# Performance work log

Measured on AMD Instinct MI355X. Metric: run time of the kernel, lower is better.

The kernel has to match this reference:

```python
import jax, jax.numpy as jnp
import numpy as np

B, L, N, CIN = 16, 12, 2048, 3
EMB, GRAP, LAYERS, OUT = 64, 16, 3, 12
SP, TID, DIW = 16, 16, 16
M = EMB + SP + TID + DIW  # model_size = 112


def setup_inputs() -> dict:
    key = jax.random.key(0)
    ks = jax.random.split(key, 12)
    s = jnp.float32(0.02)
    return {
        "history_data": jax.random.uniform(ks[0], (B, L, N, CIN), dtype=jnp.float32),
        "adj": jax.nn.softmax(jax.random.normal(ks[1], (N, N), dtype=jnp.float32), axis=1),
        "node_emb": jax.random.normal(ks[2], (N, SP), dtype=jnp.float32) * s,
        "tid_emb": jax.random.normal(ks[3], (288, TID), dtype=jnp.float32) * s,
        "diw_emb": jax.random.normal(ks[4], (7, DIW), dtype=jnp.float32) * s,
        "W_in": jax.random.normal(ks[5], (CIN, EMB), dtype=jnp.float32) * s,
        "b_in": jnp.zeros((EMB,), jnp.float32),
        "W_pre": jax.random.normal(ks[6], (M, 4 * M), dtype=jnp.float32) * s,
        "b_pre": jnp.zeros((4 * M,), jnp.float32),
        "E_dy": jax.random.normal(ks[7], (N, GRAP), dtype=jnp.float32) * s,
        "W_dy": jax.random.normal(ks[8], (M, 4 * M), dtype=jnp.float32) * s,
        "b_dy": jnp.zeros((4 * M,), jnp.float32),
        "W_dec": jax.random.normal(ks[9], (OUT, LAYERS, M), dtype=jnp.float32) * s,
        "b_dec": jnp.zeros((OUT,), jnp.float32),
        "W_out": jax.random.normal(ks[10], (OUT, OUT), dtype=jnp.float32) * s,
        "b_out": jnp.zeros((OUT,), jnp.float32),
    }


def _run_layer(hidd_t, A, W, b):
    """Graph-conv LSTM-style recurrent layer; returns last-timestep hidden [B,N,M]."""
    def step(ct, x):  # x: [B,N,M]
        xa = jnp.einsum('bkm,nk->bnm', x, A)      # adjacency message passing
        gates = xa @ W + b                         # [B,N,4M]
        i, f, g, o = jnp.split(gates, 4, axis=-1)
        ct = jax.nn.sigmoid(f) * ct + jax.nn.sigmoid(i) * jnp.tanh(g)
        ht = jax.nn.sigmoid(o) * jnp.tanh(ct)
        return ct, ht
    ct0 = jnp.zeros(hidd_t.shape[1:], hidd_t.dtype)  # [B,N,M]
    _, hts = jax.lax.scan(step, ct0, hidd_t)
    return hts[-1]


def reference(history_data, adj, node_emb, tid_emb, diw_emb, W_in, b_in,
              W_pre, b_pre, E_dy, W_dy, b_dy, W_dec, b_dec, W_out, b_out):
    Bx, Lx = history_data.shape[0], history_data.shape[1]
    # temporal embedding indices (truncating cast, matches torch LongTensor)
    t_idx = (history_data[..., 1] * 288).astype(jnp.int32)
    d_idx = (history_data[..., 2] * 7).astype(jnp.int32)
    inp = history_data @ W_in + b_in                                   # [B,L,N,EMB]
    node = jnp.broadcast_to(node_emb, (Bx, Lx) + node_emb.shape)       # [B,L,N,SP]
    hidd = jnp.concatenate([inp, node, tid_emb[t_idx], diw_emb[d_idx]], axis=-1)  # [B,L,N,M]
    hidd_t = jnp.moveaxis(hidd, 1, 0)                                  # [L,B,N,M]
    A_dy = jax.nn.softmax(jax.nn.relu(E_dy @ E_dy.T), axis=1)          # adaptive adjacency
    outs = [_run_layer(hidd_t, adj, W_pre, b_pre)]                     # layer 0: predefined graph
    for _ in range(LAYERS - 1):
        outs.append(_run_layer(hidd_t, A_dy, W_dy, b_dy))              # layers >0: dynamic graph
    final = jnp.stack(outs, axis=1)                                    # [B,LAYERS,N,M]
    # decoder Conv2d(layer_num->out_len, kernel (1,M)) then 1x1 Conv2d
    x = jnp.einsum('bznm,ozm->bon', final, W_dec) + b_dec[None, :, None]
    x = jnp.einsum('bon,po->bpn', x, W_out) + b_out[None, :, None]
    return x  # [B,OUT,N]
```

## Files before the change

kernel.cpp:

```cpp
#include <hip/hip_runtime.h>
#include <hip/hip_bf16.h>
#include <cstdint>
#include <cstddef>

typedef float f4 __attribute__((ext_vector_type(4)));
typedef short s16x8 __attribute__((ext_vector_type(8)));
typedef short s16x4 __attribute__((ext_vector_type(4)));

#define N_NODES 2048
#define BATCH 16
#define LSEQ 12
#define MDIM 112
#define GDIM 448
#define KC 35
#define NCOLS_X 6784
#define NREAL (KC*BATCH*LSEQ)
#define XROW 7680
#define KBIG 2048
#define KL 64
#define WTB_SH (GDIM * KL)

#define GLDS16(SRC, DST)                                                        \
    __builtin_amdgcn_global_load_lds(                                           \
        (const __attribute__((address_space(1))) void*)(SRC),                   \
        (__attribute__((address_space(3))) void*)(DST), 16, 0, 0)

#define MFMA16(ACC, AV, BV) \
    ACC = __builtin_amdgcn_mfma_f32_16x16x32_bf16(AV, BV, ACC, 0, 0, 0)

__device__ __forceinline__ short bf16hi(float v) {
    union { __hip_bfloat16 h; short s; } u;
    u.h = __float2bfloat16(v);
    return u.s;
}
__device__ __forceinline__ short bf16lo(float v) {
    union { __hip_bfloat16 h; short s; } u;
    u.h = __float2bfloat16(v);
    float r = v - __bfloat162float(u.h);
    u.h = __float2bfloat16(r);
    return u.s;
}
__device__ __forceinline__ float rcpf_(float x)  { return __builtin_amdgcn_rcpf(x); }
__device__ __forceinline__ float sigf_(float x)  { return rcpf_(1.0f + __expf(-x)); }
__device__ __forceinline__ float tanhf_(float x) { return 1.0f - 2.0f * rcpf_(1.0f + __expf(2.0f * x)); }

__device__ __forceinline__ float wave_sum(float v) {
#pragma unroll
    for (int off = 32; off > 0; off >>= 1) v += __shfl_down(v, off);
    return v;
}

__global__ void adaptive_adj_kernel(const float* __restrict__ E,
                                    const float* __restrict__ node_emb,
                                    __hip_bfloat16* __restrict__ Abig,
                                    float* __restrict__ node_a,
                                    float* __restrict__ rs)
{
    __shared__ float sbuf[N_NODES];
    __shared__ float red[256];
    __shared__ float part[17][4];
    const int n = blockIdx.x;
    const int tid = threadIdx.x;
    float en[16];
#pragma unroll
    for (int i = 0; i < 16; ++i) en[i] = E[n * 16 + i];
    float lmax = -3.4e38f;
    for (int k = tid; k < N_NODES; k += 256) {
        const float* ek = E + k * 16;
        float d = 0.f;
#pragma unroll
        for (int i = 0; i < 16; ++i) d += en[i] * ek[i];
        d = fmaxf(d, 0.0f);
        sbuf[k] = d;
        lmax = fmaxf(lmax, d);
    }
    red[tid] = lmax; __syncthreads();
    for (int s = 128; s > 0; s >>= 1) {
        if (tid < s) red[tid] = fmaxf(red[tid], red[tid + s]);
        __syncthreads();
    }
    float mx = red[0];
    __syncthreads();
    float lsum = 0.f;
    for (int k = tid; k < N_NODES; k += 256) {
        float e = __expf(sbuf[k] - mx);
        sbuf[k] = e;
        lsum += e;
    }
    red[tid] = lsum; __syncthreads();
    for (int s = 128; s > 0; s >>= 1) {
        if (tid < s) red[tid] += red[tid + s];
        __syncthreads();
    }
    float rinv = rcpf_(red[0]);
    __syncthreads();

    __hip_bfloat16* arow = Abig + (size_t)(2048 + n) * KBIG;
    float p[17];
#pragma unroll
    for (int i = 0; i < 17; ++i) p[i] = 0.f;
    for (int k = tid; k < N_NODES; k += 256) {
        float a = sbuf[k] * rinv;
        arow[k] = __float2bfloat16(a);
        const float* e = node_emb + k * 16;
        p[16] += a;
#pragma unroll
        for (int i = 0; i < 16; ++i) p[i] += a * e[i];
    }
#pragma unroll
    for (int e = 0; e < 17; ++e) {
        float v = wave_sum(p[e]);
        if ((tid & 63) == 0) part[e][tid >> 6] = v;
    }
    __syncthreads();
    if (tid < 17) {
        float s = part[tid][0] + part[tid][1] + part[tid][2] + part[tid][3];
        if (tid < 16) node_a[n * 16 + tid] = s;
        else rs[n] = s;
    }
}

__global__ void node_rs_kernel(const float* __restrict__ A,
                               const float* __restrict__ node_emb,
                               float* __restrict__ node_a, float* __restrict__ rs)
{
    __shared__ float part[17][4];
    const int n = blockIdx.x;
    const int tid = threadIdx.x;
    float p[17];
#pragma unroll
    for (int i = 0; i < 17; ++i) p[i] = 0.f;
    for (int k = tid; k < N_NODES; k += 256) {
        float a = A[(size_t)n * N_NODES + k];
        const float* e = node_emb + k * 16;
        p[16] += a;
#pragma unroll
        for (int i = 0; i < 16; ++i) p[i] += a * e[i];
    }
#pragma unroll
    for (int e = 0; e < 17; ++e) {
        float v = wave_sum(p[e]);
        if ((tid & 63) == 0) part[e][tid >> 6] = v;
    }
    __syncthreads();
    if (tid < 17) {
        float s = part[tid][0] + part[tid][1] + part[tid][2] + part[tid][3];
        if (tid < 16) node_a[n * 16 + tid] = s;
        else rs[n] = s;
    }
}

__global__ void wtb_pack_kernel(const float* __restrict__ W_in,
                                const float* __restrict__ b_in,
                                const float* __restrict__ Wp,
                                const float* __restrict__ bp,
                                const float* __restrict__ Wd,
                                const float* __restrict__ bd,
                                short* __restrict__ outp)
{
    int idx = blockIdx.x * 256 + threadIdx.x;
    if (idx >= 2 * GDIM * KL) return;
    int z = idx >= GDIM * KL;
    int rem = idx - z * GDIM * KL;
    const float* W  = z ? Wd : Wp;
    const float* bg = z ? bd : bp;
    int p = rem & 63;
    int r = rem >> 6;
    int tile = r >> 4, gc = r & 15;
    int mi = tile >> 2, co = tile & 3;
    int g = co * 112 + mi * 16 + gc;

    float v = 0.f; bool lo = false; bool zero = false;
    #define DOTW(VEC) ({ float s_ = 0.f;                                     \
        for (int m = 0; m < 64; ++m) s_ += (VEC)[m] * W[(size_t)m * GDIM + g];\
        s_; })
    if (p < 3)         v = DOTW(W_in + p * 64);
    else if (p < 35)   v = W[(size_t)(80 + p - 3) * GDIM + g];
    else if (p < 38)   v = DOTW(W_in + (p - 35) * 64);
    else if (p < 41) { v = DOTW(W_in + (p - 38) * 64); lo = true; }
    else if (p == 41)  v = bg[g];
    else if (p == 42)  v = DOTW(b_in);
    else if (p < 59)   v = W[(size_t)(64 + p - 43) * GDIM + g];
    else if (p == 59) { v = bg[g]; lo = true; }
    else if (p == 60) { v = DOTW(b_in); lo = true; }
    else zero = true;
    #undef DOTW
    short s = zero ? (short)0 : (lo ? bf16lo(v) : bf16hi(v));
    int a = r * 128 + p * 2;
    int asw = a ^ (((a >> 7) & 7) << 4);
    outp[(size_t)z * WTB_SH + (asw >> 1)] = s;
}

#define AQUADS (2048 * 2048 / 4)
#define XQUADS (NCOLS_X * 2048 / 4)
__global__ void pack_build_kernel(const float* __restrict__ adj,
                                  const float* __restrict__ hist,
                                  const float* __restrict__ tid_emb,
                                  const float* __restrict__ diw_emb,
                                  __hip_bfloat16* __restrict__ Abig,
                                  __hip_bfloat16* __restrict__ XT)
{
    int idx = blockIdx.x * 256 + threadIdx.x;
    if (idx < AQUADS) {
        int e0 = idx << 2;
        int k = e0 & 2047;
        int m = e0 >> 11;
        f4 v = *(const f4*)(adj + (size_t)m * 2048 + k);
        s16x4 o = { bf16hi(v[0]), bf16hi(v[1]), bf16hi(v[2]), bf16hi(v[3]) };
        *(s16x4*)((short*)Abig + (size_t)m * KBIG + k) = o;
        return;
    }
    int xi = idx - AQUADS;
    if (xi >= XQUADS) return;
    int e0 = xi << 2;
    int k0 = e0 & 2047;
    int jl = e0 >> 11;
    s16x4 o = {0, 0, 0, 0};
    if (jl < NREAL) {
        int c = jl % KC;
        int bl = jl / KC;
#pragma unroll
        for (int i = 0; i < 4; ++i) {
            const float* h = hist + ((size_t)(bl * N_NODES + k0 + i)) * 3;
            float v;
            if (c < 3) v = h[c];
            else if (c < 19) { int ti = (int)(h[1] * 288.0f); v = tid_emb[ti * 16 + (c - 3)]; }
            else             { int di = (int)(h[2] * 7.0f);   v = diw_emb[di * 16 + (c - 19)]; }
            o[i] = bf16hi(v);
        }
    }
    *(s16x4*)((short*)XT + (size_t)jl * KBIG + k0) = o;
}

__global__ __launch_bounds__(512, 4) void gemm_bf16_kernel(const short* __restrict__ A,
                                                           const short* __restrict__ BT,
                                                           short* __restrict__ XAhi)
{
    __shared__ short As[256 * 64];
    __shared__ short Bs[128 * 64];
    const int tid = threadIdx.x;
    const int w = tid >> 6;
    const int l = tid & 63;
    const int wr = w >> 1;
    const int wc = w & 1;
    const int lm = l & 15;

    const int bid = blockIdx.y * 53 + blockIdx.x;
    const int sid = (bid & 7) * 106 + (bid >> 3);
    const int col = sid >> 4;
    const int row = sid & 15;
    const int m0 = row * 256;
    const int jt = col * 128;

    const int srow = tid >> 3;
    const int koct = (tid & 7) ^ (srow & 7);
    const size_t gA = (size_t)(m0 + srow) * KBIG + koct * 8;
    const size_t gB = (size_t)(jt + srow) * KBIG + koct * 8;
    char* lA = (char*)As + srow * 128 + (tid & 7) * 16;
    char* lB = (char*)Bs + srow * 128 + (tid & 7) * 16;

    f4 acc[4][4];
#pragma unroll
    for (int i = 0; i < 4; ++i)
#pragma unroll
        for (int j = 0; j < 4; ++j)
#pragma unroll
            for (int e = 0; e < 4; ++e) acc[i][j][e] = 0.f;

    const int sm  = (l & 7) << 4;
    const int k16 = (l >> 4) * 16;

    for (int kt = 0; kt < KBIG; kt += 64) {
        __syncthreads();
        GLDS16(A  + gA + kt,                      lA);
        GLDS16(A  + gA + kt + (size_t)64  * KBIG, lA + 64  * 128);
        GLDS16(A  + gA + kt + (size_t)128 * KBIG, lA + 128 * 128);
        GLDS16(A  + gA + kt + (size_t)192 * KBIG, lA + 192 * 128);
        GLDS16(BT + gB + kt,                      lB);
        GLDS16(BT + gB + kt + (size_t)64  * KBIG, lB + 64  * 128);
        __syncthreads();
#pragma unroll
        for (int ks = 0; ks < 2; ++ks) {
            const int ko = (ks * 64 + k16) ^ sm;
            s16x8 a[4], b[4];
#pragma unroll
            for (int mi = 0; mi < 4; ++mi)
                a[mi] = *(const s16x8*)((const char*)As + (wr * 64 + mi * 16 + lm) * 128 + ko);
#pragma unroll
            for (int ni = 0; ni < 4; ++ni)
                b[ni] = *(const s16x8*)((const char*)Bs + (wc * 64 + ni * 16 + lm) * 128 + ko);
#pragma unroll
            for (int mi = 0; mi < 4; ++mi)
#pragma unroll
                for (int ni = 0; ni < 4; ++ni)
                    MFMA16(acc[mi][ni], a[mi], b[ni]);
        }
    }

    const int rbase = m0 + wr * 64 + (l >> 4) * 4;
    const int cbase = jt + wc * 64 + lm;
#pragma unroll
    for (int mi = 0; mi < 4; ++mi)
#pragma unroll
        for (int ni = 0; ni < 4; ++ni) {
            int cc = cbase + ni * 16;
            if (cc < NREAL) {
                int bt = cc / KC;
                int c  = cc - bt * KC;
#pragma unroll
                for (int reg = 0; reg < 4; ++reg) {
                    size_t roff = (size_t)(rbase + mi * 16 + reg) * XROW;
                    float v = acc[mi][ni][reg];
                    XAhi[roff + (size_t)bt * 40 + c] = bf16hi(v);
                    if (c < 3) XAhi[roff + (size_t)bt * 40 + 36 + c] = bf16lo(v);
                }
            }
        }
}

__global__ __launch_bounds__(512, 4) void lstm6_kernel(
    const short* __restrict__ XAhi,
    const short* __restrict__ WtBg,
    const float* __restrict__ na_pre, const float* __restrict__ na_dy,
    const float* __restrict__ rs_pre, const float* __restrict__ rs_dy,
    float* __restrict__ H)
{
    __shared__ short sWtb[WTB_SH];
    __shared__ short sXa[128 * KL];
    const int tid = threadIdx.x;
    const int w = tid >> 6, l = tid & 63;
    const int n0 = blockIdx.x * 128;
    const int b  = blockIdx.y;
    const int z  = blockIdx.z;
    const float* na = z ? na_dy : na_pre;
    const float* rs = z ? rs_dy : rs_pre;

    {
        const char* gW = (const char*)(WtBg + (size_t)z * WTB_SH);
        char* lW = (char*)sWtb;
        for (int it = 0; it < 7; ++it) {
            int base = (it * 8 + w) * 64;
            GLDS16(gW + (size_t)(base + l) * 16, lW + base * 16);
        }
    }

    const int sr = tid & 127;
    const int pp = tid >> 7;
    const short* xarow = XAhi + (size_t)(z * 2048 + n0 + sr) * XROW;
    const float* narow = na + (size_t)(n0 + sr) * 16;
    const float rsv = rs[n0 + sr];
    char* wrow = (char*)sXa + sr * 128;
    const int wswz = (sr & 7) << 4;

    const int lm = l & 15;
    const int sm = (l & 7) << 4;
    const int kof0 = ((l >> 4) * 16) ^ sm;
    const int kof1 = (64 + (l >> 4) * 16) ^ sm;
    const int an = w * 16 + lm;
    const char* xab = (const char*)sXa;
    const char* wtbb = (const char*)sWtb;
    float* Hout = H + (size_t)z * BATCH * N_NODES * MDIM;

    float cc[7][4];
#pragma unroll
    for (int mi = 0; mi < 7; ++mi)
#pragma unroll
        for (int q = 0; q < 4; ++q) cc[mi][q] = 0.f;

    s16x8 ph0 = {0,0,0,0,0,0,0,0}, ph1 = ph0;
    s16x4 p0 = {0,0,0,0}, p32 = p0, plo = p0;
    {
        const int bt = b * LSEQ;
        if (pp < 2) {
            ph0 = *(const s16x8*)(xarow + bt * 40 + pp * 16);
            ph1 = *(const s16x8*)(xarow + bt * 40 + pp * 16 + 8);
        } else if (pp == 2) {
            p0  = *(const s16x4*)(xarow + bt * 40);
            p32 = *(const s16x4*)(xarow + bt * 40 + 32);
            plo = *(const s16x4*)(xarow + bt * 40 + 36);
        }
    }

    for (int t = 0; t < LSEQ; ++t) {
        __syncthreads();
        if (pp < 2) {
            *(s16x8*)(wrow + ((pp * 32 + 0)  ^ wswz)) = ph0;
            *(s16x8*)(wrow + ((pp * 32 + 16) ^ wswz)) = ph1;
        } else if (pp == 2) {
            short v[16];
            v[0] = p32[0]; v[1] = p32[1]; v[2] = p32[2];
            v[3] = plo[0]; v[4] = plo[1]; v[5] = plo[2];
            v[6] = p0[0];  v[7] = p0[1];  v[8] = p0[2];
            v[9]  = bf16hi(1.0f);
            v[10] = bf16hi(rsv);
#pragma unroll
            for (int j = 11; j < 16; ++j) v[j] = bf16hi(narow[j - 11]);
#pragma unroll
            for (int q = 0; q < 4; ++q) {
                s16x4 sv = { v[q * 4], v[q * 4 + 1], v[q * 4 + 2], v[q * 4 + 3] };
                *(s16x4*)(wrow + ((2 * 32 + q * 8) ^ wswz)) = sv;
            }
        } else {
            short v[16];
#pragma unroll
            for (int j = 0; j < 11; ++j) v[j] = bf16hi(narow[5 + j]);
            v[11] = bf16hi(1.0f);
            v[12] = bf16hi(rsv);
            v[13] = 0; v[14] = 0; v[15] = 0;
#pragma unroll
            for (int q = 0; q < 4; ++q) {
                s16x4 sv = { v[q * 4], v[q * 4 + 1], v[q * 4 + 2], v[q * 4 + 3] };
                *(s16x4*)(wrow + ((3 * 32 + q * 8) ^ wswz)) = sv;
            }
        }
        __syncthreads();

        if (t + 1 < LSEQ) {
            const int bt = b * LSEQ + t + 1;
            if (pp < 2) {
                ph0 = *(const s16x8*)(xarow + bt * 40 + pp * 16);
                ph1 = *(const s16x8*)(xarow + bt * 40 + pp * 16 + 8);
            } else if (pp == 2) {
                p0  = *(const s16x4*)(xarow + bt * 40);
                p32 = *(const s16x4*)(xarow + bt * 40 + 32);
                plo = *(const s16x4*)(xarow + bt * 40 + 36);
            }
        }

        s16x8 a0 = *(const s16x8*)(xab + an * 128 + kof0);
        s16x8 a1 = *(const s16x8*)(xab + an * 128 + kof1);
#pragma unroll
        for (int mi = 0; mi < 7; ++mi) {
            const char* bb = wtbb + (mi * 64 + lm) * 128;
            f4 gi = {0.f, 0.f, 0.f, 0.f};
            f4 gf = gi, gg = gi;
            MFMA16(gi, a0, *(const s16x8*)(bb + kof0));
            MFMA16(gi, a1, *(const s16x8*)(bb + kof1));
            MFMA16(gf, a0, *(const s16x8*)(bb + 2048 + kof0));
            MFMA16(gf, a1, *(const s16x8*)(bb + 2048 + kof1));
            MFMA16(gg, a0, *(const s16x8*)(bb + 4096 + kof0));
            MFMA16(gg, a1, *(const s16x8*)(bb + 4096 + kof1));
#pragma unroll
            for (int q = 0; q < 4; ++q) {
                float si = sigf_(gi[q]);
                float sf = sigf_(gf[q]);
                float tg = tanhf_(gg[q]);
                cc[mi][q] = sf * cc[mi][q] + si * tg;
            }
            if (t == LSEQ - 1) {
                f4 go = {0.f, 0.f, 0.f, 0.f};
                MFMA16(go, a0, *(const s16x8*)(bb + 6144 + kof0));
                MFMA16(go, a1, *(const s16x8*)(bb + 6144 + kof1));
#pragma unroll
                for (int q = 0; q < 4; ++q) {
                    float h = sigf_(go[q]) * tanhf_(cc[mi][q]);
                    Hout[((size_t)b * N_NODES + n0 + w * 16 + (l >> 4) * 4 + q) * MDIM
                         + mi * 16 + lm] = h;
                }
            }
        }
    }
}

__global__ void decode_kernel(const float* __restrict__ H,
                              const float* __restrict__ Wdec,
                              const float* __restrict__ bdec,
                              const float* __restrict__ Wout,
                              const float* __restrict__ bout,
                              float* __restrict__ out)
{
    int g = blockIdx.x * 256 + threadIdx.x;
    if (g >= BATCH * N_NODES) return;
    int b = g >> 11;
    int n = g & 2047;
    const f4* h0 = (const f4*)(H + (size_t)g * MDIM);
    const f4* h1 = (const f4*)(H + (size_t)BATCH * N_NODES * MDIM + (size_t)g * MDIM);
    float x[12];
#pragma unroll
    for (int o = 0; o < 12; ++o) x[o] = bdec[o];
    for (int mq = 0; mq < 28; ++mq) {
        f4 a0 = h0[mq], a1 = h1[mq];
#pragma unroll
        for (int e = 0; e < 4; ++e) {
            int m = mq * 4 + e;
#pragma unroll
            for (int o = 0; o < 12; ++o)
                x[o] += a0[e] * Wdec[(o * 3 + 0) * MDIM + m]
                      + a1[e] * (Wdec[(o * 3 + 1) * MDIM + m] + Wdec[(o * 3 + 2) * MDIM + m]);
        }
    }
#pragma unroll
    for (int p = 0; p < 12; ++p) {
        float s = bout[p];
#pragma unroll
        for (int o = 0; o < 12; ++o) s += Wout[p * 12 + o] * x[o];
        out[((size_t)b * 12 + p) * N_NODES + n] = s;
    }
}

extern "C" void kernel_launch(void* const* d_in, const int* in_sizes, int n_in,
                              void* d_out, int out_size, void* d_ws, size_t ws_size,
                              hipStream_t stream)
{
    const float* hist   = (const float*)d_in[0];
    const float* adj    = (const float*)d_in[1];
    const float* node_e = (const float*)d_in[2];
    const float* tid_e  = (const float*)d_in[3];
    const float* diw_e  = (const float*)d_in[4];
    const float* W_in   = (const float*)d_in[5];
    const float* b_in   = (const float*)d_in[6];
    const float* W_pre  = (const float*)d_in[7];
    const float* b_pre  = (const float*)d_in[8];
    const float* E_dy   = (const float*)d_in[9];
    const float* W_dy   = (const float*)d_in[10];
    const float* b_dy   = (const float*)d_in[11];
    const float* W_dec  = (const float*)d_in[12];
    const float* b_dec  = (const float*)d_in[13];
    const float* W_out  = (const float*)d_in[14];
    const float* b_out  = (const float*)d_in[15];
    float* out = (float*)d_out;

    float* ws = (float*)d_ws;
    const size_t XAHI_F = (size_t)4096 * XROW / 2;
    const size_t ABIG_F = (size_t)4096 * KBIG / 2;
    const size_t XT_F   = (size_t)NCOLS_X * KBIG / 2;

    short* XAhi  = (short*)ws;
    float* AbigF = ws + XAHI_F;
    __hip_bfloat16* Abig = (__hip_bfloat16*)AbigF;
    float* H     = AbigF;
    __hip_bfloat16* XTc = (__hip_bfloat16*)(ws + XAHI_F + ABIG_F);
    float* tail = ws + XAHI_F + ABIG_F + XT_F;
    float* na_pre = tail;                     tail += (size_t)N_NODES * 16;
    float* na_dy  = tail;                     tail += (size_t)N_NODES * 16;
    float* rs_pre = tail;                     tail += N_NODES;
    float* rs_dy  = tail;                     tail += N_NODES;
    short* WtBg   = (short*)tail;

    adaptive_adj_kernel<<<N_NODES, 256, 0, stream>>>(E_dy, node_e, Abig, na_dy, rs_dy);
    node_rs_kernel<<<N_NODES, 256, 0, stream>>>(adj, node_e, na_pre, rs_pre);
    wtb_pack_kernel<<<(2 * GDIM * KL + 255) / 256, 256, 0, stream>>>(
        W_in, b_in, W_pre, b_pre, W_dy, b_dy, WtBg);

    pack_build_kernel<<<(AQUADS + XQUADS + 255) / 256, 256, 0, stream>>>(
        adj, hist, tid_e, diw_e, Abig, XTc);

    gemm_bf16_kernel<<<dim3(53, 16), 512, 0, stream>>>(
        (const short*)Abig, (const short*)XTc, XAhi);

    lstm6_kernel<<<dim3(N_NODES / 128, BATCH, 2), 512, 0, stream>>>(
        XAhi, WtBg, na_pre, na_dy, rs_pre, rs_dy, H);

    decode_kernel<<<(BATCH * N_NODES + 255) / 256, 256, 0, stream>>>(
        H, W_dec, b_dec, W_out, b_out, out);
}
```

Before: 319.0 us.

## Fold node-embedding and row-sum reductions into the big adjacency GEMM padding columns

Removes the separate node_rs_kernel and the per-row node_emb/rowsum reductions from adaptive_adj_kernel. Instead, the otherwise-zero padding columns of the packed X matrix now hold node_emb (split into hi and lo bf16 parts) and a ones column, so the existing bf16 GEMM computes A·node_emb and the row sums for free. The last column tile writes these into na/rs buffers. This saves a full fp32 pass over the 2048x2048 adj matrix and extra launches. In exchange the row sums come from the bf16-rounded adjacency, which changes numerics slightly.

After: 283.2 us, median of 3. 1.13x faster.

```diff
diff --git a/kernel.cpp b/kernel.cpp
--- a/kernel.cpp
+++ b/kernel.cpp
@@ -15,6 +15,9 @@
 #define KC 35
 #define NCOLS_X 6784
 #define NREAL (KC*BATCH*LSEQ)
+#define NA_HI 6720
+#define NA_LO 6736
+#define RS_COL 6752
 #define XROW 7680
 #define KBIG 2048
 #define KL 64
@@ -44,21 +47,11 @@
 __device__ __forceinline__ float sigf_(float x)  { return rcpf_(1.0f + __expf(-x)); }
 __device__ __forceinline__ float tanhf_(float x) { return 1.0f - 2.0f * rcpf_(1.0f + __expf(2.0f * x)); }
 
-__device__ __forceinline__ float wave_sum(float v) {
-#pragma unroll
-    for (int off = 32; off > 0; off >>= 1) v += __shfl_down(v, off);
-    return v;
-}
-
 __global__ void adaptive_adj_kernel(const float* __restrict__ E,
-                                    const float* __restrict__ node_emb,
-                                    __hip_bfloat16* __restrict__ Abig,
-                                    float* __restrict__ node_a,
-                                    float* __restrict__ rs)
+                                    __hip_bfloat16* __restrict__ Abig)
 {
     __shared__ float sbuf[N_NODES];
     __shared__ float red[256];
-    __shared__ float part[17][4];
     const int n = blockIdx.x;
     const int tid = threadIdx.x;
     float en[16];
@@ -96,58 +89,8 @@
     __syncthreads();
 
     __hip_bfloat16* arow = Abig + (size_t)(2048 + n) * KBIG;
-    float p[17];
-#pragma unroll
-    for (int i = 0; i < 17; ++i) p[i] = 0.f;
-    for (int k = tid; k < N_NODES; k += 256) {
-        float a = sbuf[k] * rinv;
-        arow[k] = __float2bfloat16(a);
-        const float* e = node_emb + k * 16;
-        p[16] += a;
-#pragma unroll
-        for (int i = 0; i < 16; ++i) p[i] += a * e[i];
-    }
-#pragma unroll
-    for (int e = 0; e < 17; ++e) {
-        float v = wave_sum(p[e]);
-        if ((tid & 63) == 0) part[e][tid >> 6] = v;
-    }
-    __syncthreads();
-    if (tid < 17) {
-        float s = part[tid][0] + part[tid][1] + part[tid][2] + part[tid][3];
-        if (tid < 16) node_a[n * 16 + tid] = s;
-        else rs[n] = s;
-    }
-}
-
-__global__ void node_rs_kernel(const float* __restrict__ A,
-                               const float* __restrict__ node_emb,
-                               float* __restrict__ node_a, float* __restrict__ rs)
-{
-    __shared__ float part[17][4];
-    const int n = blockIdx.x;
-    const int tid = threadIdx.x;
-    float p[17];
-#pragma unroll
-    for (int i = 0; i < 17; ++i) p[i] = 0.f;
-    for (int k = tid; k < N_NODES; k += 256) {
-        float a = A[(size_t)n * N_NODES + k];
-        const float* e = node_emb + k * 16;
-        p[16] += a;
-#pragma unroll
-        for (int i = 0; i < 16; ++i) p[i] += a * e[i];
-    }
-#pragma unroll
-    for (int e = 0; e < 17; ++e) {
-        float v = wave_sum(p[e]);
-        if ((tid & 63) == 0) part[e][tid >> 6] = v;
-    }
-    __syncthreads();
-    if (tid < 17) {
-        float s = part[tid][0] + part[tid][1] + part[tid][2] + part[tid][3];
-        if (tid < 16) node_a[n * 16 + tid] = s;
-        else rs[n] = s;
-    }
+    for (int k = tid; k < N_NODES; k += 256)
+        arow[k] = __float2bfloat16(sbuf[k] * rinv);
 }
 
 __global__ void wtb_pack_kernel(const float* __restrict__ W_in,
@@ -197,6 +140,7 @@
                                   const float* __restrict__ hist,
                                   const float* __restrict__ tid_emb,
                                   const float* __restrict__ diw_emb,
+                                  const float* __restrict__ node_emb,
                                   __hip_bfloat16* __restrict__ Abig,
                                   __hip_bfloat16* __restrict__ XT)
 {
@@ -228,13 +172,28 @@
             else             { int di = (int)(h[2] * 7.0f);   v = diw_emb[di * 16 + (c - 19)]; }
             o[i] = bf16hi(v);
         }
+    } else if (jl >= NA_HI && jl < NA_LO) {
+        int e = jl - NA_HI;
+#pragma unroll
+        for (int i = 0; i < 4; ++i) o[i] = bf16hi(node_emb[(k0 + i) * 16 + e]);
+    } else if (jl >= NA_LO && jl < RS_COL) {
+        int e = jl - NA_LO;
+#pragma unroll
+        for (int i = 0; i < 4; ++i) o[i] = bf16lo(node_emb[(k0 + i) * 16 + e]);
+    } else if (jl == RS_COL) {
+        short one = bf16hi(1.0f);
+        o[0] = one; o[1] = one; o[2] = one; o[3] = one;
     }
     *(s16x4*)((short*)XT + (size_t)jl * KBIG + k0) = o;
 }
 
 __global__ __launch_bounds__(512, 4) void gemm_bf16_kernel(const short* __restrict__ A,
                                                            const short* __restrict__ BT,
-                                                           short* __restrict__ XAhi)
+                                                           short* __restrict__ XAhi,
+                                                           float* __restrict__ na_pre,
+                                                           float* __restrict__ na_dy,
+                                                           float* __restrict__ rs_pre,
+                                                           float* __restrict__ rs_dy)
 {
     __shared__ short As[256 * 64];
     __shared__ short Bs[128 * 64];
@@ -316,6 +275,24 @@
                 }
             }
         }
+
+    if (jt == 6656 && wc == 1) {
+#pragma unroll
+        for (int mi = 0; mi < 4; ++mi)
+#pragma unroll
+            for (int reg = 0; reg < 4; ++reg) {
+                int r = rbase + mi * 16 + reg;
+                float nav = acc[mi][0][reg] + acc[mi][1][reg];
+                int rr = r & 2047;
+                if (r < 2048) {
+                    na_pre[rr * 16 + lm] = nav;
+                    if (lm == 0) rs_pre[rr] = acc[mi][2][reg];
+                } else {
+                    na_dy[rr * 16 + lm] = nav;
+                    if (lm == 0) rs_dy[rr] = acc[mi][2][reg];
+                }
+            }
+    }
 }
 
 __global__ __launch_bounds__(512, 4) void lstm6_kernel(
@@ -537,16 +514,15 @@
     float* rs_dy  = tail;                     tail += N_NODES;
     short* WtBg   = (short*)tail;
 
-    adaptive_adj_kernel<<<N_NODES, 256, 0, stream>>>(E_dy, node_e, Abig, na_dy, rs_dy);
-    node_rs_kernel<<<N_NODES, 256, 0, stream>>>(adj, node_e, na_pre, rs_pre);
+    adaptive_adj_kernel<<<N_NODES, 256, 0, stream>>>(E_dy, Abig);
     wtb_pack_kernel<<<(2 * GDIM * KL + 255) / 256, 256, 0, stream>>>(
         W_in, b_in, W_pre, b_pre, W_dy, b_dy, WtBg);
 
     pack_build_kernel<<<(AQUADS + XQUADS + 255) / 256, 256, 0, stream>>>(
-        adj, hist, tid_e, diw_e, Abig, XTc);
+        adj, hist, tid_e, diw_e, node_e, Abig, XTc);
 
     gemm_bf16_kernel<<<dim3(53, 16), 512, 0, stream>>>(
-        (const short*)Abig, (const short*)XTc, XAhi);
+        (const short*)Abig, (const short*)XTc, XAhi, na_pre, na_dy, rs_pre, rs_dy);
 
     lstm6_kernel<<<dim3(N_NODES / 128, BATCH, 2), 512, 0, stream>>>(
         XAhi, WtBg, na_pre, na_dy, rs_pre, rs_dy, H);
```
